# Optimization experiments

Hardware: AMD Instinct MI355X
Metric: run time of the kernel (lower is better)

## Reference

```python
import jax, jax.numpy as jnp
import numpy as np
import math

N_EMBD = 512
N_HEAD = 8
B, T = 2, 4096


def setup_inputs() -> dict:
    key = jax.random.key(0)
    ks = jax.random.split(key, 12)
    s = 1.0 / math.sqrt(N_EMBD)
    inp = {
        "x": jax.random.normal(ks[0], (B, T, N_EMBD), dtype=jnp.float32),
        "weight": jax.random.uniform(ks[1], (1,), dtype=jnp.float32),
        "state": jax.random.uniform(ks[2], (1,), dtype=jnp.float32),
        "Wq": jax.random.normal(ks[3], (N_EMBD, N_EMBD), dtype=jnp.float32) * s,
        "bq": jnp.zeros((N_EMBD,), dtype=jnp.float32),
        "Wk": jax.random.normal(ks[4], (N_EMBD, N_EMBD), dtype=jnp.float32) * s,
        "bk": jnp.zeros((N_EMBD,), dtype=jnp.float32),
        "Wv": jax.random.normal(ks[5], (N_EMBD, N_EMBD), dtype=jnp.float32) * s,
        "bv": jnp.zeros((N_EMBD,), dtype=jnp.float32),
        "Wp": jax.random.normal(ks[6], (N_EMBD, N_EMBD), dtype=jnp.float32) * s,
        "bp": jnp.zeros((N_EMBD,), dtype=jnp.float32),
    }
    return inp


def reference(x, weight, state, Wq, bq, Wk, bk, Wv, bv, Wp, bp):
    # weight / state are accepted but unused, matching the torch module.
    Bb, Tt, C = x.shape
    hd = C // N_HEAD

    def split_heads(t):  # [B,T,C] -> [B,H,T,hd]
        return t.reshape(Bb, Tt, N_HEAD, hd).transpose(0, 2, 1, 3)

    # torch nn.Linear: y = x @ W.T + b
    q = split_heads(x @ Wq.T + bq)
    k = split_heads(x @ Wk.T + bk)
    v = split_heads(x @ Wv.T + bv)

    scale = 1.0 / math.sqrt(hd)
    att = jnp.einsum("bhqd,bhkd->bhqk", q, k) * scale  # [B,H,T,T]
    causal = jnp.tril(jnp.ones((Tt, Tt), dtype=bool))
    att = jnp.where(causal[None, None, :, :], att, -jnp.inf)
    att = jax.nn.softmax(att, axis=-1)
    # attn_drop / resid_drop are identity (p=0 / eval)
    y = jnp.einsum("bhqk,bhkd->bhqd", att, v)  # [B,H,T,hd]
    y = y.transpose(0, 2, 1, 3).reshape(Bb, Tt, C)
    return y @ Wp.T + bp
```

## Files before the change

kernel.cpp:

```cpp
#include <hip/hip_runtime.h>
#include <math.h>

using short8  = __attribute__((ext_vector_type(8))) short;
using floatx4 = __attribute__((ext_vector_type(4))) float;

#define DEVI __device__ __forceinline__

#define BATCH 2
#define SEQ   4096
#define NE    512
#define NH    8
#define HD    64
#define MTOT  8192

#define QSCALE 0.18033688011112042f

DEVI short f2bf(float f) {
    unsigned u = __builtin_bit_cast(unsigned, f);
    unsigned r = (u + 0x7fffu + ((u >> 16) & 1u)) >> 16;
    return (short)r;
}

DEVI void async16(const void* g, void* l) {
    __builtin_amdgcn_global_load_lds(
        (const __attribute__((address_space(1))) void*)g,
        (__attribute__((address_space(3))) void*)l, 16, 0, 0);
}

__global__ __launch_bounds__(256) void cvt_bf16(const float* __restrict__ src,
                                                short* __restrict__ dst, int n4) {
    int i = blockIdx.x * 256 + threadIdx.x;
    if (i >= n4) return;
    float4 f = ((const float4*)src)[i];
    short4 o;
    o.x = f2bf(f.x); o.y = f2bf(f.y); o.z = f2bf(f.z); o.w = f2bf(f.w);
    ((short4*)dst)[i] = o;
}

DEVI void gemm_mainloop(const short* __restrict__ A, const short* __restrict__ W,
                        int m0, int n0, short* ldsA, short* ldsW, floatx4 (&acc)[4][4]) {
    const int tid  = threadIdx.x;
    const int lane = tid & 63;
    const int w    = tid >> 6;
    const int wm   = w >> 1, wn = w & 1;
    const int quad = lane >> 4, l15 = lane & 15;
    const int srow = lane >> 3, scol = (lane & 7) * 8;

    for (int i = 0; i < 4; ++i)
        for (int j = 0; j < 4; ++j)
            acc[i][j] = floatx4{0.f, 0.f, 0.f, 0.f};

    for (int kt = 0; kt < NE / 64; ++kt) {
        const int k0 = kt * 64;
        for (int c = 0; c < 4; ++c) {
            const int rb = w * 32 + c * 8;
            async16(A + (size_t)(m0 + rb + srow) * NE + k0 + scol, ldsA + rb * 64);
            async16(W + (size_t)(n0 + rb + srow) * NE + k0 + scol, ldsW + rb * 64);
        }
        __syncthreads();
        for (int ks = 0; ks < 2; ++ks) {
            short8 af[4], bf[4];
            for (int i = 0; i < 4; ++i)
                af[i] = *(const short8*)(ldsA + (wm * 64 + i * 16 + l15) * 64 + ks * 32 + quad * 8);
            for (int j = 0; j < 4; ++j)
                bf[j] = *(const short8*)(ldsW + (wn * 64 + j * 16 + l15) * 64 + ks * 32 + quad * 8);
            for (int i = 0; i < 4; ++i)
                for (int j = 0; j < 4; ++j)
                    acc[i][j] = __builtin_amdgcn_mfma_f32_16x16x32_bf16(af[i], bf[j], acc[i][j], 0, 0, 0);
        }
        __syncthreads();
    }
}

__global__ __launch_bounds__(256) void gemm_qkv(const short* __restrict__ xbf,
                                                const short* __restrict__ wbf,
                                                const float* __restrict__ bq,
                                                const float* __restrict__ bk,
                                                const float* __restrict__ bv,
                                                short* __restrict__ qkv) {
    __shared__ short ldsA[128 * 64];
    __shared__ short ldsW[128 * 64];
    const int m0 = blockIdx.x * 128, n0 = blockIdx.y * 128, z = blockIdx.z;
    const short* W = wbf + (size_t)z * (NE * NE);
    const float* bias = (z == 0) ? bq : (z == 1) ? bk : bv;
    short* out = qkv + (size_t)z * (MTOT * NE);

    floatx4 acc[4][4];
    gemm_mainloop(xbf, W, m0, n0, ldsA, ldsW, acc);

    const int lane = threadIdx.x & 63, w = threadIdx.x >> 6;
    const int wm = w >> 1, wn = w & 1, quad = lane >> 4, l15 = lane & 15;
    const float scale = (z == 0) ? QSCALE : 1.0f;
    for (int j = 0; j < 4; ++j) {
        const int col = n0 + wn * 64 + j * 16 + l15;
        const float bz = bias[col];
        const int h = col >> 6, d = col & 63;
        for (int i = 0; i < 4; ++i) {
            for (int r = 0; r < 4; ++r) {
                const int row = m0 + wm * 64 + i * 16 + quad * 4 + r;
                const int b = row >> 12, t = row & 4095;
                const float v = (acc[i][j][r] + bz) * scale;
                out[(((size_t)(b * NH + h)) * SEQ + t) * HD + d] = f2bf(v);
            }
        }
    }
}

__global__ __launch_bounds__(256) void transpose_v(const short* __restrict__ vb,
                                                   short* __restrict__ vt) {
    const int bh = blockIdx.y;
    const int t0 = blockIdx.x * 64;
    __shared__ short tile[64 * 66];
    const int tid = threadIdx.x;
    const int r  = tid >> 3;
    const int c8 = tid & 7;

    const short* src = vb + ((size_t)bh * SEQ + t0) * HD;
#pragma unroll
    for (int p = 0; p < 2; ++p) {
        const int row = p * 32 + r;
        short8 v = *(const short8*)&src[row * HD + c8 * 8];
#pragma unroll
        for (int i = 0; i < 8; ++i)
            tile[row * 66 + c8 * 8 + i] = v[i];
    }
    __syncthreads();

    short* dst = vt + (size_t)bh * (HD * SEQ) + t0;
#pragma unroll
    for (int p = 0; p < 2; ++p) {
        const int d = p * 32 + r;
        short8 o;
#pragma unroll
        for (int i = 0; i < 8; ++i)
            o[i] = tile[(c8 * 8 + i) * 66 + d];
        *(short8*)&dst[(size_t)d * SEQ + c8 * 8] = o;
    }
}

__global__ __launch_bounds__(256) void gemm_proj(const short* __restrict__ ybf,
                                                 const short* __restrict__ wp,
                                                 const float* __restrict__ bp,
                                                 float* __restrict__ out) {
    __shared__ short ldsA[128 * 64];
    __shared__ short ldsW[128 * 64];
    const int m0 = blockIdx.x * 128, n0 = blockIdx.y * 128;

    floatx4 acc[4][4];
    gemm_mainloop(ybf, wp, m0, n0, ldsA, ldsW, acc);

    const int lane = threadIdx.x & 63, w = threadIdx.x >> 6;
    const int wm = w >> 1, wn = w & 1, quad = lane >> 4, l15 = lane & 15;
    for (int j = 0; j < 4; ++j) {
        const int col = n0 + wn * 64 + j * 16 + l15;
        const float bz = bp[col];
        for (int i = 0; i < 4; ++i) {
            for (int r = 0; r < 4; ++r) {
                const int row = m0 + wm * 64 + i * 16 + quad * 4 + r;
                out[(size_t)row * NE + col] = acc[i][j][r] + bz;
            }
        }
    }
}

__global__ __launch_bounds__(256, 2) void attn(const short* __restrict__ q,
                                               const short* __restrict__ k,
                                               const short* __restrict__ vt,
                                               short* __restrict__ y) {
    const int id = blockIdx.x;
    const int bx = id >> 4;
    const int bh = ((id & 7) << 1) | ((id >> 3) & 1);
    const int tid = threadIdx.x, lane = tid & 63, w = tid >> 6;
    const int quad = lane >> 4, l15 = lane & 15;

    __shared__ short ldsK[2][64 * 64];
    __shared__ short ldsV[2][64 * 64];
    __shared__ short ldsP[4][16 * 72];

    const short* K  = k  + (size_t)bh * (SEQ * HD);
    const short* VT = vt + (size_t)bh * (HD * SEQ);
    short* myP = (short*)ldsP[w];
    const int b = bh >> 3, h = bh & 7;

    const int lb   = ((lane & 7) - (lane >> 3)) & 7;
    const int jrow = lane >> 3;
    const int p0 = (quad + (l15 & 7)) & 7;
    const int p1 = p0 ^ 4;

    for (int sel = 0; sel < 2; ++sel) {
        const int qt = sel ? (SEQ / 64 - 1 - bx) : bx;
        const short* Q = q + (size_t)bh * (SEQ * HD) + (size_t)qt * 64 * HD;

        short8 qfrag[2];
#pragma unroll
        for (int ks = 0; ks < 2; ++ks)
            qfrag[ks] = *(const short8*)&Q[(w * 16 + l15) * HD + ks * 32 + quad * 8];

        floatx4 O[4];
        float lsum[4];
#pragma unroll
        for (int n = 0; n < 4; ++n) O[n] = floatx4{0.f, 0.f, 0.f, 0.f};
#pragma unroll
        for (int r = 0; r < 4; ++r) lsum[r] = 0.f;

        __syncthreads();
#pragma unroll
        for (int c2 = 0; c2 < 2; ++c2) {
            const int chunk = w * 2 + c2;
            const int j = chunk * 8 + jrow;
            async16(K + (size_t)j * HD + lb * 8, ldsK[0] + chunk * 512);
            async16(VT + (size_t)j * SEQ + lb * 8, ldsV[0] + chunk * 512);
        }

        for (int jt = 0; jt <= qt; ++jt) {
            __syncthreads();
            const int cur = jt & 1;

            if (jt < qt) {
                const int nx = cur ^ 1;
                const short* Kt = K + (size_t)(jt + 1) * 64 * HD;
                const short* Vc = VT + (jt + 1) * 64;
#pragma unroll
                for (int c2 = 0; c2 < 2; ++c2) {
                    const int chunk = w * 2 + c2;
                    const int j = chunk * 8 + jrow;
                    async16(Kt + (size_t)j * HD + lb * 8, ldsK[nx] + chunk * 512);
                    async16(Vc + (size_t)j * SEQ + lb * 8, ldsV[nx] + chunk * 512);
                }
            }

            const short* bK = ldsK[cur];
            const short* bV = ldsV[cur];
            short8 kf[2][4], vf[2][4];
#pragma unroll
            for (int n = 0; n < 4; ++n) {
                const int row = n * 16 + l15;
                kf[0][n] = *(const short8*)(bK + row * 64 + p0 * 8);
                kf[1][n] = *(const short8*)(bK + row * 64 + p1 * 8);
                vf[0][n] = *(const short8*)(bV + row * 64 + p0 * 8);
                vf[1][n] = *(const short8*)(bV + row * 64 + p1 * 8);
            }

            floatx4 S[4];
#pragma unroll
            for (int n = 0; n < 4; ++n) S[n] = floatx4{0.f, 0.f, 0.f, 0.f};
#pragma unroll
            for (int ks = 0; ks < 2; ++ks)
#pragma unroll
                for (int n = 0; n < 4; ++n)
                    S[n] = __builtin_amdgcn_mfma_f32_16x16x32_bf16(qfrag[ks], kf[ks][n], S[n], 0, 0, 0);

            if (jt == qt) {
#pragma unroll
                for (int n = 0; n < 4; ++n)
#pragma unroll
                    for (int r = 0; r < 4; ++r) {
                        const int rowl = w * 16 + quad * 4 + r;
                        const int coll = n * 16 + l15;
                        if (coll > rowl) S[n][r] = -3.0e38f;
                    }
            }

#pragma unroll
            for (int n = 0; n < 4; ++n)
#pragma unroll
                for (int r = 0; r < 4; ++r)
                    S[n][r] = __builtin_amdgcn_exp2f(S[n][r]);
#pragma unroll
            for (int r = 0; r < 4; ++r)
                lsum[r] += (S[0][r] + S[1][r]) + (S[2][r] + S[3][r]);

#pragma unroll
            for (int n = 0; n < 4; ++n)
#pragma unroll
                for (int r = 0; r < 4; ++r)
                    myP[(quad * 4 + r) * 72 + n * 16 + l15] = f2bf(S[n][r]);

            short8 pf[2];
#pragma unroll
            for (int ks = 0; ks < 2; ++ks)
                pf[ks] = *(const short8*)(myP + l15 * 72 + ks * 32 + quad * 8);

#pragma unroll
            for (int ks = 0; ks < 2; ++ks)
#pragma unroll
                for (int n = 0; n < 4; ++n)
                    O[n] = __builtin_amdgcn_mfma_f32_16x16x32_bf16(pf[ks], vf[ks][n], O[n], 0, 0, 0);
        }

#pragma unroll
        for (int r = 0; r < 4; ++r) {
#pragma unroll
            for (int off = 1; off < 16; off <<= 1)
                lsum[r] += __shfl_xor(lsum[r], off, 64);
        }

#pragma unroll
        for (int r = 0; r < 4; ++r) {
            const float inv = 1.0f / lsum[r];
            const int t = qt * 64 + w * 16 + quad * 4 + r;
#pragma unroll
            for (int n = 0; n < 4; ++n) {
                const int col = h * 64 + n * 16 + l15;
                y[((size_t)(b * SEQ + t)) * NE + col] = f2bf(O[n][r] * inv);
            }
        }
    }
}

extern "C" void kernel_launch(void* const* d_in, const int* in_sizes, int n_in,
                              void* d_out, int out_size, void* d_ws, size_t ws_size,
                              hipStream_t stream) {
    const float* x  = (const float*)d_in[0];
    const float* Wq = (const float*)d_in[3];
    const float* bq = (const float*)d_in[4];
    const float* Wk = (const float*)d_in[5];
    const float* bk = (const float*)d_in[6];
    const float* Wv = (const float*)d_in[7];
    const float* bv = (const float*)d_in[8];
    const float* Wp = (const float*)d_in[9];
    const float* bp = (const float*)d_in[10];
    float* out = (float*)d_out;

    short* ws   = (short*)d_ws;
    short* xbf  = ws;
    short* wbf  = xbf + (size_t)MTOT * NE;
    short* qb   = wbf + 4 * (size_t)NE * NE;
    short* kb   = qb + (size_t)MTOT * NE;
    short* vb   = kb + (size_t)MTOT * NE;
    short* vtb  = xbf;
    short* yb   = vb;

    cvt_bf16<<<(MTOT * NE / 4 + 255) / 256, 256, 0, stream>>>(x, xbf, MTOT * NE / 4);
    cvt_bf16<<<(NE * NE / 4 + 255) / 256, 256, 0, stream>>>(Wq, wbf + 0 * (size_t)NE * NE, NE * NE / 4);
    cvt_bf16<<<(NE * NE / 4 + 255) / 256, 256, 0, stream>>>(Wk, wbf + 1 * (size_t)NE * NE, NE * NE / 4);
    cvt_bf16<<<(NE * NE / 4 + 255) / 256, 256, 0, stream>>>(Wv, wbf + 2 * (size_t)NE * NE, NE * NE / 4);
    cvt_bf16<<<(NE * NE / 4 + 255) / 256, 256, 0, stream>>>(Wp, wbf + 3 * (size_t)NE * NE, NE * NE / 4);

    gemm_qkv<<<dim3(MTOT / 128, NE / 128, 3), 256, 0, stream>>>(xbf, wbf, bq, bk, bv, qb);

    transpose_v<<<dim3(SEQ / 64, BATCH * NH), 256, 0, stream>>>(vb, vtb);

    attn<<<dim3(512), 256, 0, stream>>>(qb, kb, vtb, yb);

    gemm_proj<<<dim3(MTOT / 128, NE / 128), 256, 0, stream>>>(yb, wbf + 3 * (size_t)NE * NE, bp, out);
}
```

Measured before the change: 211.9 us.

## Process KV tiles in pairs per barrier and fuse bf16 conversion launches

After: 201.2 us. 5.1% less time.

```diff
diff --git a/kernel.cpp b/kernel.cpp
--- a/kernel.cpp
+++ b/kernel.cpp
@@ -27,14 +27,28 @@
         (__attribute__((address_space(3))) void*)l, 16, 0, 0);
 }
 
-__global__ __launch_bounds__(256) void cvt_bf16(const float* __restrict__ src,
-                                                short* __restrict__ dst, int n4) {
+__global__ __launch_bounds__(256) void cvt_all(const float* __restrict__ x,
+                                               const float* __restrict__ wq,
+                                               const float* __restrict__ wk,
+                                               const float* __restrict__ wv,
+                                               const float* __restrict__ wp,
+                                               short* __restrict__ xbf,
+                                               short* __restrict__ wbf) {
     int i = blockIdx.x * 256 + threadIdx.x;
-    if (i >= n4) return;
-    float4 f = ((const float4*)src)[i];
+    const float* src; short* dst; int off;
+    if (i < MTOT * NE / 4) {
+        src = x; dst = xbf; off = i;
+    } else {
+        int j = i - MTOT * NE / 4;
+        int wsel = j >> 16;
+        off = j & 65535;
+        src = (wsel == 0) ? wq : (wsel == 1) ? wk : (wsel == 2) ? wv : wp;
+        dst = wbf + (size_t)wsel * NE * NE;
+    }
+    float4 f = ((const float4*)src)[off];
     short4 o;
     o.x = f2bf(f.x); o.y = f2bf(f.y); o.z = f2bf(f.z); o.w = f2bf(f.w);
-    ((short4*)dst)[i] = o;
+    ((short4*)dst)[off] = o;
 }
 
 DEVI void gemm_mainloop(const short* __restrict__ A, const short* __restrict__ W,
@@ -173,8 +187,8 @@
     const int tid = threadIdx.x, lane = tid & 63, w = tid >> 6;
     const int quad = lane >> 4, l15 = lane & 15;
 
-    __shared__ short ldsK[2][64 * 64];
-    __shared__ short ldsV[2][64 * 64];
+    __shared__ short ldsK[2][2][64 * 64];
+    __shared__ short ldsV[2][2][64 * 64];
     __shared__ short ldsP[4][16 * 72];
 
     const short* K  = k  + (size_t)bh * (SEQ * HD);
@@ -203,89 +217,111 @@
 #pragma unroll
         for (int r = 0; r < 4; ++r) lsum[r] = 0.f;
 
+        const int npair = (qt >> 1) + 1;
+
         __syncthreads();
 #pragma unroll
-        for (int c2 = 0; c2 < 2; ++c2) {
-            const int chunk = w * 2 + c2;
-            const int j = chunk * 8 + jrow;
-            async16(K + (size_t)j * HD + lb * 8, ldsK[0] + chunk * 512);
-            async16(VT + (size_t)j * SEQ + lb * 8, ldsV[0] + chunk * 512);
-        }
-
-        for (int jt = 0; jt <= qt; ++jt) {
-            __syncthreads();
-            const int cur = jt & 1;
-
-            if (jt < qt) {
-                const int nx = cur ^ 1;
-                const short* Kt = K + (size_t)(jt + 1) * 64 * HD;
-                const short* Vc = VT + (jt + 1) * 64;
+        for (int s = 0; s < 2; ++s) {
+            const int js = s;
+            if (js <= qt) {
+                const short* Kt = K + (size_t)js * 64 * HD;
+                const short* Vc = VT + js * 64;
 #pragma unroll
                 for (int c2 = 0; c2 < 2; ++c2) {
                     const int chunk = w * 2 + c2;
                     const int j = chunk * 8 + jrow;
-                    async16(Kt + (size_t)j * HD + lb * 8, ldsK[nx] + chunk * 512);
-                    async16(Vc + (size_t)j * SEQ + lb * 8, ldsV[nx] + chunk * 512);
+                    async16(Kt + (size_t)j * HD + lb * 8, ldsK[0][s] + chunk * 512);
+                    async16(Vc + (size_t)j * SEQ + lb * 8, ldsV[0][s] + chunk * 512);
                 }
             }
-
-            const short* bK = ldsK[cur];
-            const short* bV = ldsV[cur];
-            short8 kf[2][4], vf[2][4];
-#pragma unroll
-            for (int n = 0; n < 4; ++n) {
-                const int row = n * 16 + l15;
-                kf[0][n] = *(const short8*)(bK + row * 64 + p0 * 8);
-                kf[1][n] = *(const short8*)(bK + row * 64 + p1 * 8);
-                vf[0][n] = *(const short8*)(bV + row * 64 + p0 * 8);
-                vf[1][n] = *(const short8*)(bV + row * 64 + p1 * 8);
-            }
-
-            floatx4 S[4];
-#pragma unroll
-            for (int n = 0; n < 4; ++n) S[n] = floatx4{0.f, 0.f, 0.f, 0.f};
-#pragma unroll
-            for (int ks = 0; ks < 2; ++ks)
+        }
+
+        for (int p = 0; p < npair; ++p) {
+            __syncthreads();
+            const int pipe = p & 1;
+
+            if (p + 1 < npair) {
+                const int nx = pipe ^ 1;
+#pragma unroll
+                for (int s = 0; s < 2; ++s) {
+                    const int js = 2 * (p + 1) + s;
+                    if (js <= qt) {
+                        const short* Kt = K + (size_t)js * 64 * HD;
+                        const short* Vc = VT + js * 64;
+#pragma unroll
+                        for (int c2 = 0; c2 < 2; ++c2) {
+                            const int chunk = w * 2 + c2;
+                            const int j = chunk * 8 + jrow;
+                            async16(Kt + (size_t)j * HD + lb * 8, ldsK[nx][s] + chunk * 512);
+                            async16(Vc + (size_t)j * SEQ + lb * 8, ldsV[nx][s] + chunk * 512);
+                        }
+                    }
+                }
+            }
+
+#pragma unroll
+            for (int s = 0; s < 2; ++s) {
+                const int jt = 2 * p + s;
+                if (jt > qt) break;
+
+                const short* bK = ldsK[pipe][s];
+                const short* bV = ldsV[pipe][s];
+                short8 kf[2][4], vf[2][4];
+#pragma unroll
+                for (int n = 0; n < 4; ++n) {
+                    const int row = n * 16 + l15;
+                    kf[0][n] = *(const short8*)(bK + row * 64 + p0 * 8);
+                    kf[1][n] = *(const short8*)(bK + row * 64 + p1 * 8);
+                    vf[0][n] = *(const short8*)(bV + row * 64 + p0 * 8);
+                    vf[1][n] = *(const short8*)(bV + row * 64 + p1 * 8);
+                }
+
+                floatx4 S[4];
+#pragma unroll
+                for (int n = 0; n < 4; ++n) S[n] = floatx4{0.f, 0.f, 0.f, 0.f};
+#pragma unroll
+                for (int ks = 0; ks < 2; ++ks)
+#pragma unroll
+                    for (int n = 0; n < 4; ++n)
+                        S[n] = __builtin_amdgcn_mfma_f32_16x16x32_bf16(qfrag[ks], kf[ks][n], S[n], 0, 0, 0);
+
+                if (jt == qt) {
+#pragma unroll
+                    for (int n = 0; n < 4; ++n)
+#pragma unroll
+                        for (int r = 0; r < 4; ++r) {
+                            const int rowl = w * 16 + quad * 4 + r;
+                            const int coll = n * 16 + l15;
+                            if (coll > rowl) S[n][r] = -3.0e38f;
+                        }
+                }
+
 #pragma unroll
                 for (int n = 0; n < 4; ++n)
-                    S[n] = __builtin_amdgcn_mfma_f32_16x16x32_bf16(qfrag[ks], kf[ks][n], S[n], 0, 0, 0);
-
-            if (jt == qt) {
+#pragma unroll
+                    for (int r = 0; r < 4; ++r)
+                        S[n][r] = __builtin_amdgcn_exp2f(S[n][r]);
+#pragma unroll
+                for (int r = 0; r < 4; ++r)
+                    lsum[r] += (S[0][r] + S[1][r]) + (S[2][r] + S[3][r]);
+
 #pragma unroll
                 for (int n = 0; n < 4; ++n)
 #pragma unroll
-                    for (int r = 0; r < 4; ++r) {
-                        const int rowl = w * 16 + quad * 4 + r;
-                        const int coll = n * 16 + l15;
-                        if (coll > rowl) S[n][r] = -3.0e38f;
-                    }
-            }
-
-#pragma unroll
-            for (int n = 0; n < 4; ++n)
-#pragma unroll
-                for (int r = 0; r < 4; ++r)
-                    S[n][r] = __builtin_amdgcn_exp2f(S[n][r]);
-#pragma unroll
-            for (int r = 0; r < 4; ++r)
-                lsum[r] += (S[0][r] + S[1][r]) + (S[2][r] + S[3][r]);
-
-#pragma unroll
-            for (int n = 0; n < 4; ++n)
-#pragma unroll
-                for (int r = 0; r < 4; ++r)
-                    myP[(quad * 4 + r) * 72 + n * 16 + l15] = f2bf(S[n][r]);
-
-            short8 pf[2];
-#pragma unroll
-            for (int ks = 0; ks < 2; ++ks)
-                pf[ks] = *(const short8*)(myP + l15 * 72 + ks * 32 + quad * 8);
-
-#pragma unroll
-            for (int ks = 0; ks < 2; ++ks)
-#pragma unroll
-                for (int n = 0; n < 4; ++n)
-                    O[n] = __builtin_amdgcn_mfma_f32_16x16x32_bf16(pf[ks], vf[ks][n], O[n], 0, 0, 0);
+                    for (int r = 0; r < 4; ++r)
+                        myP[(quad * 4 + r) * 72 + n * 16 + l15] = f2bf(S[n][r]);
+
+                short8 pf[2];
+#pragma unroll
+                for (int ks = 0; ks < 2; ++ks)
+                    pf[ks] = *(const short8*)(myP + l15 * 72 + ks * 32 + quad * 8);
+
+#pragma unroll
+                for (int ks = 0; ks < 2; ++ks)
+#pragma unroll
+                    for (int n = 0; n < 4; ++n)
+                        O[n] = __builtin_amdgcn_mfma_f32_16x16x32_bf16(pf[ks], vf[ks][n], O[n], 0, 0, 0);
+            }
         }
 
 #pragma unroll
@@ -331,11 +367,8 @@
     short* vtb  = xbf;
     short* yb   = vb;
 
-    cvt_bf16<<<(MTOT * NE / 4 + 255) / 256, 256, 0, stream>>>(x, xbf, MTOT * NE / 4);
-    cvt_bf16<<<(NE * NE / 4 + 255) / 256, 256, 0, stream>>>(Wq, wbf + 0 * (size_t)NE * NE, NE * NE / 4);
-    cvt_bf16<<<(NE * NE / 4 + 255) / 256, 256, 0, stream>>>(Wk, wbf + 1 * (size_t)NE * NE, NE * NE / 4);
-    cvt_bf16<<<(NE * NE / 4 + 255) / 256, 256, 0, stream>>>(Wv, wbf + 2 * (size_t)NE * NE, NE * NE / 4);
-    cvt_bf16<<<(NE * NE / 4 + 255) / 256, 256, 0, stream>>>(Wp, wbf + 3 * (size_t)NE * NE, NE * NE / 4);
+    cvt_all<<<dim3((MTOT * NE / 4 + 4 * NE * NE / 4) / 256), 256, 0, stream>>>(
+        x, Wq, Wk, Wv, Wp, xbf, wbf);
 
     gemm_qkv<<<dim3(MTOT / 128, NE / 128, 3), 256, 0, stream>>>(xbf, wbf, bq, bk, bv, qb);
 
```
